# Optimization experiments

Hardware: AMD Instinct MI355X
Metric: run time of the kernel (lower is better)

## Reference

```python
import jax, jax.numpy as jnp
import numpy as np

D_MODEL = 1024
N_HEAD = 16
B, T = 4, 1024
MAX_REL = 32  # max_relative_positions


def setup_inputs() -> dict:
    key = jax.random.key(0)
    ks = jax.random.split(key, 12)
    s = 0.02
    inp = {
        "x": jax.random.normal(ks[0], (B, T, D_MODEL), jnp.float32),
        "mask": jnp.tril(jnp.ones((T, T), dtype=bool)),  # causal mask, 1 = keep
        "Wq": jax.random.normal(ks[1], (D_MODEL, D_MODEL), jnp.float32) * s,
        "bq": jax.random.normal(ks[2], (D_MODEL,), jnp.float32) * s,
        "Wk": jax.random.normal(ks[3], (D_MODEL, D_MODEL), jnp.float32) * s,
        "bk": jax.random.normal(ks[4], (D_MODEL,), jnp.float32) * s,
        "Wv": jax.random.normal(ks[5], (D_MODEL, D_MODEL), jnp.float32) * s,
        "bv": jax.random.normal(ks[6], (D_MODEL,), jnp.float32) * s,
        "Wo": jax.random.normal(ks[7], (D_MODEL, D_MODEL), jnp.float32) * s,
        "bo": jax.random.normal(ks[8], (D_MODEL,), jnp.float32) * s,
        "rel_bias": jax.random.normal(ks[9], (2 * MAX_REL - 1, N_HEAD), jnp.float32) * s,
        "n_head": N_HEAD,
    }
    return inp


def reference(x, mask, Wq, bq, Wk, bk, Wv, bv, Wo, bo, rel_bias, n_head):
    Bx, Tx, C = x.shape
    Dh = C // n_head
    scale = Dh ** (-0.5)
    # projections: torch Linear is x @ W.T + b
    Q = (x @ Wq.T + bq).reshape(Bx, Tx, n_head, Dh)
    K = (x @ Wk.T + bk).reshape(Bx, Tx, n_head, Dh)
    V = (x @ Wv.T + bv).reshape(Bx, Tx, n_head, Dh)
    # scores: [B, H, T, T]
    scores = jnp.einsum("bqhd,bkhd->bhqk", Q, K) * scale
    # T5-style clipped relative-position bias
    pos = jnp.arange(Tx)
    rel = pos[None, :] - pos[:, None]                     # k_pos - q_pos, [T, T]
    buckets = jnp.clip(rel, -(MAX_REL - 1), MAX_REL - 1) + (MAX_REL - 1)
    bias = rel_bias[buckets]                              # [T, T, H]
    scores = scores + jnp.transpose(bias, (2, 0, 1))[None]
    # original applies masked_fill(-inf) then masked_fill(0): net effect = 0
    scores = jnp.where(mask, scores, 0.0)
    w = jax.nn.relu(scores) + 1e-6
    w = jnp.where(mask, w, 0.0)
    w = w / (jnp.sum(w, axis=-1, keepdims=True) + 1e-6)
    out = jnp.einsum("bhqk,bkhd->bqhd", w, V).reshape(Bx, Tx, C)
    return out @ Wo.T + bo
```

## Files before the change

### kernel.cpp

```cpp
#include <hip/hip_runtime.h>


typedef __attribute__((ext_vector_type(8))) __bf16 bf16x8;
typedef __attribute__((ext_vector_type(4))) __bf16 bf16x4;
typedef __attribute__((ext_vector_type(4))) float f32x4;
typedef unsigned short u16;

__device__ __forceinline__ u16 f2bf(float f) {
  unsigned u = __float_as_uint(f);
  u += 0x7FFFu + ((u >> 16) & 1u);
  return (u16)(u >> 16);
}
__device__ __forceinline__ float bf2f(u16 b) {
  return __uint_as_float(((unsigned)b) << 16);
}
__device__ __forceinline__ void gl_lds16(const void* g, void* l) {
  __builtin_amdgcn_global_load_lds((__attribute__((address_space(1))) void*)g,
                                   (__attribute__((address_space(3))) void*)l,
                                   16, 0, 0);
}

__global__ __launch_bounds__(256) void cast_all_kernel(
    const float* __restrict__ x,  const float* __restrict__ wq,
    const float* __restrict__ wk, const float* __restrict__ wv,
    const float* __restrict__ wo,
    u16* __restrict__ xb, u16* __restrict__ wqb, u16* __restrict__ wkb,
    u16* __restrict__ wvb, u16* __restrict__ wob) {
  long i4 = (long)blockIdx.x * 256 + threadIdx.x;
  const float* src; u16* dst; long rel;
  if (i4 < 1048576) { src = x; dst = xb; rel = i4; }
  else {
    long j = i4 - 1048576;
    int w = (int)(j >> 18);
    rel = j & 262143;
    src = (w == 0) ? wq : (w == 1) ? wk : (w == 2) ? wv : wo;
    dst = (w == 0) ? wqb : (w == 1) ? wkb : (w == 2) ? wvb : wob;
  }
  float4 v = ((const float4*)src)[rel];
  ushort4 o;
  o.x = f2bf(v.x); o.y = f2bf(v.y); o.z = f2bf(v.z); o.w = f2bf(v.w);
  ((ushort4*)dst)[rel] = o;
}

__global__ __launch_bounds__(256) void gemm_qkv(
    const u16* __restrict__ xb, const u16* __restrict__ wqb,
    const u16* __restrict__ wkb, const u16* __restrict__ wvb,
    const float* __restrict__ bq, const float* __restrict__ bk,
    const float* __restrict__ bv,
    u16* __restrict__ Qb, u16* __restrict__ Kb, u16* __restrict__ Vtg) {
  constexpr int K = 1024;
  __shared__ __align__(16) u16 As[128 * 64];
  __shared__ __align__(16) u16 Bs[128 * 64];

  const int bx = blockIdx.x;
  const u16 *AT, *BT;
  const float* bias;
  u16* C;
  int m0, n0, ldc;
  bool rowbias;
  if (bx < 512) {
    int g = bx >> 5;
    int sel = g >> 3;
    n0 = (g & 7) * 128; m0 = (bx & 31) * 128;
    AT = xb; BT = sel ? wkb : wqb; bias = sel ? bk : bq;
    C = sel ? Kb : Qb; ldc = 1024; rowbias = false;
  } else {
    int rem = bx - 512;
    n0 = (rem >> 3) * 128; m0 = (rem & 7) * 128;
    AT = wvb; BT = xb; bias = bv;
    C = Vtg; ldc = 4096; rowbias = true;
  }

  const int t = threadIdx.x;
  const int lane = t & 63;
  const int wv = t >> 6;
  const int quad = lane >> 4;
  const int l15 = lane & 15;
  const int wr = wv >> 1, wc = wv & 1;

  const f32x4 vzero = {0.f, 0.f, 0.f, 0.f};
  f32x4 acc[4][4];
#pragma unroll
  for (int i = 0; i < 4; ++i)
#pragma unroll
    for (int j = 0; j < 4; ++j) acc[i][j] = vzero;

  for (int kt = 0; kt < K / 64; ++kt) {
    const int k0 = kt * 64;
#pragma unroll
    for (int p = 0; p < 4; ++p) {
      int idx = t + p * 256;
      int row = idx >> 3, seg = idx & 7;
      gl_lds16(&AT[(long)(m0 + row) * K + k0 + seg * 8], &As[idx * 8]);
      gl_lds16(&BT[(long)(n0 + row) * K + k0 + seg * 8], &Bs[idx * 8]);
    }
    __syncthreads();
#pragma unroll
    for (int ks = 0; ks < 64; ks += 32) {
      bf16x8 af[4], bfg[4];
#pragma unroll
      for (int i = 0; i < 4; ++i)
        af[i] = *(const bf16x8*)&As[(wr * 64 + i * 16 + l15) * 64 + ks + quad * 8];
#pragma unroll
      for (int j = 0; j < 4; ++j)
        bfg[j] = *(const bf16x8*)&Bs[(wc * 64 + j * 16 + l15) * 64 + ks + quad * 8];
#pragma unroll
      for (int i = 0; i < 4; ++i)
#pragma unroll
        for (int j = 0; j < 4; ++j)
          acc[i][j] = __builtin_amdgcn_mfma_f32_16x16x32_bf16(af[i], bfg[j], acc[i][j], 0, 0, 0);
    }
    __syncthreads();
  }

  float cb[4];
  if (!rowbias) {
#pragma unroll
    for (int j = 0; j < 4; ++j) cb[j] = bias[n0 + wc * 64 + j * 16 + l15];
  }

#pragma unroll
  for (int i = 0; i < 4; ++i) {
#pragma unroll
    for (int r = 0; r < 4; ++r) {
      int row = m0 + wr * 64 + i * 16 + quad * 4 + r;
      long base = (long)row * ldc + n0 + wc * 64;
      float rb_ = rowbias ? bias[row] : 0.f;
#pragma unroll
      for (int j = 0; j < 4; ++j) {
        float v = acc[i][j][r] + (rowbias ? rb_ : cb[j]);
        C[base + j * 16 + l15] = f2bf(v);
      }
    }
  }
}

__global__ __launch_bounds__(256) void gemm_out(
    const u16* __restrict__ A, const u16* __restrict__ B,
    const float* __restrict__ bias, float* __restrict__ C) {
  constexpr int K = 1024;
  __shared__ __align__(16) u16 As[128 * 64];
  __shared__ __align__(16) u16 Bs[128 * 64];

  const int m0 = blockIdx.x * 128;
  const int n0 = blockIdx.y * 128;

  const int t = threadIdx.x;
  const int lane = t & 63;
  const int wv = t >> 6;
  const int quad = lane >> 4;
  const int l15 = lane & 15;
  const int wr = wv >> 1, wc = wv & 1;

  const f32x4 vzero = {0.f, 0.f, 0.f, 0.f};
  f32x4 acc[4][4];
#pragma unroll
  for (int i = 0; i < 4; ++i)
#pragma unroll
    for (int j = 0; j < 4; ++j) acc[i][j] = vzero;

  for (int kt = 0; kt < K / 64; ++kt) {
    const int k0 = kt * 64;
#pragma unroll
    for (int p = 0; p < 4; ++p) {
      int idx = t + p * 256;
      int row = idx >> 3, seg = idx & 7;
      gl_lds16(&A[(long)(m0 + row) * K + k0 + seg * 8], &As[idx * 8]);
      gl_lds16(&B[(long)(n0 + row) * K + k0 + seg * 8], &Bs[idx * 8]);
    }
    __syncthreads();
#pragma unroll
    for (int ks = 0; ks < 64; ks += 32) {
      bf16x8 af[4], bfg[4];
#pragma unroll
      for (int i = 0; i < 4; ++i)
        af[i] = *(const bf16x8*)&As[(wr * 64 + i * 16 + l15) * 64 + ks + quad * 8];
#pragma unroll
      for (int j = 0; j < 4; ++j)
        bfg[j] = *(const bf16x8*)&Bs[(wc * 64 + j * 16 + l15) * 64 + ks + quad * 8];
#pragma unroll
      for (int i = 0; i < 4; ++i)
#pragma unroll
        for (int j = 0; j < 4; ++j)
          acc[i][j] = __builtin_amdgcn_mfma_f32_16x16x32_bf16(af[i], bfg[j], acc[i][j], 0, 0, 0);
    }
    __syncthreads();
  }

  float cb[4];
#pragma unroll
  for (int j = 0; j < 4; ++j) cb[j] = bias[n0 + wc * 64 + j * 16 + l15];

#pragma unroll
  for (int i = 0; i < 4; ++i) {
#pragma unroll
    for (int r = 0; r < 4; ++r) {
      int row = m0 + wr * 64 + i * 16 + quad * 4 + r;
      long base = (long)row * 1024 + n0 + wc * 64;
#pragma unroll
      for (int j = 0; j < 4; ++j)
        C[base + j * 16 + l15] = acc[i][j][r] + cb[j];
    }
  }
}

__global__ __launch_bounds__(256) void attn_split(
    const u16* __restrict__ Qb,
    const u16* __restrict__ Kb,
    const u16* __restrict__ Vtg,
    const float* __restrict__ rel_bias,
    u16* __restrict__ att,
    u16* __restrict__ Opart,
    float* __restrict__ Dpart) {
  constexpr int WS = 68;
  __shared__ __align__(16) u16 Kt[64 * 64];
  __shared__ __align__(16) u16 Vt[64 * 64];
  __shared__ __align__(16) u16 Ws[4][16 * WS];
  __shared__ float biasl[64];

  const int bx = blockIdx.x;
  const int bh = bx / 24;
  const int slot = bx - bh * 24;
  const int b = bh >> 4, h = bh & 15;

  int qb, cbeg, cend, pidx;
  bool multi;
  if (slot < 8) { qb = slot; cbeg = 0; cend = qb; multi = false; pidx = 0; }
  else {
    int s = slot - 8;
    qb = 8 + (s >> 1);
    int part = s & 1;
    multi = true;
    pidx = (bh * 8 + (qb - 8)) * 2 + part;
    if (part == 0) { cbeg = 0; cend = 7; }
    else           { cbeg = 8; cend = qb; }
  }
  const int q0 = qb * 64;

  const int t = threadIdx.x;
  const int lane = t & 63;
  const int wv = t >> 6;
  const int quad = lane >> 4;
  const int l15 = lane & 15;

  if (t < 63) biasl[t] = rel_bias[t * 16 + h];
  const float b0c = rel_bias[h];

  const long qrow = (long)(b * 1024 + q0 + wv * 16 + l15) * 1024 + h * 64;
  bf16x8 qf0 = *(const bf16x8*)&Qb[qrow + quad * 8];
  bf16x8 qf1 = *(const bf16x8*)&Qb[qrow + 32 + quad * 8];

  const f32x4 vzero = {0.f, 0.f, 0.f, 0.f};
  f32x4 acc_o[4];
#pragma unroll
  for (int j = 0; j < 4; ++j) acc_o[j] = vzero;
  float denom = 0.f;
  const float scale = 0.125f;
  const int ql = q0 + wv * 16 + l15;
  const int sw0 = (quad ^ (l15 & 7)) * 8;
  const int sw1 = ((4 + quad) ^ (l15 & 7)) * 8;

  for (int c = cbeg; c <= cend; ++c) {
    const int k0 = c * 64;
    if (c != cbeg) __syncthreads();
#pragma unroll
    for (int p = 0; p < 2; ++p) {
      int idx = t + p * 256;
      int row = idx >> 3, seg = idx & 7;
      int sw = row * 64 + ((seg ^ (row & 7)) * 8);
      uint4 kv = *(const uint4*)&Kb[(long)(b * 1024 + k0 + row) * 1024 + h * 64 + seg * 8];
      uint4 vv = *(const uint4*)&Vtg[(long)(h * 64 + row) * 4096 + b * 1024 + k0 + seg * 8];
      *(uint4*)&Kt[sw] = kv;
      *(uint4*)&Vt[sw] = vv;
    }
    __syncthreads();

    const bool fast = (c <= qb - 2);
#pragma unroll
    for (int g = 0; g < 4; ++g) {
      const u16* kr = &Kt[(g * 16 + l15) * 64];
      bf16x8 kf0 = *(const bf16x8*)&kr[sw0];
      bf16x8 kf1 = *(const bf16x8*)&kr[sw1];
      f32x4 sT = vzero;
      sT = __builtin_amdgcn_mfma_f32_16x16x32_bf16(kf0, qf0, sT, 0, 0, 0);
      sT = __builtin_amdgcn_mfma_f32_16x16x32_bf16(kf1, qf1, sT, 0, 0, 0);
      const int kgb = k0 + g * 16 + quad * 4;
      ushort4 wpk;
      if (fast) {
#pragma unroll
        for (int r = 0; r < 4; ++r) {
          float w = fmaxf(sT[r] * scale + b0c, 0.f) + 1e-6f;
          u16 wb = f2bf(w);
          denom += bf2f(wb);
          ((u16*)&wpk)[r] = wb;
        }
      } else {
#pragma unroll
        for (int r = 0; r < 4; ++r) {
          int kg = kgb + r;
          int dd = kg - ql;
          dd = dd < -31 ? -31 : (dd > 31 ? 31 : dd);
          float sv = sT[r] * scale + biasl[dd + 31];
          float w = (kg <= ql) ? (fmaxf(sv, 0.f) + 1e-6f) : 0.f;
          u16 wb = f2bf(w);
          denom += bf2f(wb);
          ((u16*)&wpk)[r] = wb;
        }
      }
      *(ushort4*)&Ws[wv][l15 * WS + g * 16 + quad * 4] = wpk;
    }
    asm volatile("s_waitcnt lgkmcnt(0)" ::: "memory");
#pragma unroll
    for (int ks = 0; ks < 64; ks += 32) {
      union { bf16x8 v8; bf16x4 v4[2]; } au;
      int wbase = l15 * WS + ks + quad * 8;
      au.v4[0] = *(const bf16x4*)&Ws[wv][wbase];
      au.v4[1] = *(const bf16x4*)&Ws[wv][wbase + 4];
      const int sv = ks ? sw1 : sw0;
#pragma unroll
      for (int j = 0; j < 4; ++j) {
        bf16x8 bvv = *(const bf16x8*)&Vt[(j * 16 + l15) * 64 + sv];
        acc_o[j] = __builtin_amdgcn_mfma_f32_16x16x32_bf16(au.v8, bvv, acc_o[j], 0, 0, 0);
      }
    }
  }

  denom += __shfl_xor(denom, 16);
  denom += __shfl_xor(denom, 32);

  if (!multi) {
    float invm = 1.f / (denom + 1e-6f);
    float inv[4];
#pragma unroll
    for (int r = 0; r < 4; ++r) inv[r] = __shfl(invm, quad * 4 + r);
#pragma unroll
    for (int j = 0; j < 4; ++j)
#pragma unroll
      for (int r = 0; r < 4; ++r) {
        int q = q0 + wv * 16 + quad * 4 + r;
        att[(long)(b * 1024 + q) * 1024 + h * 64 + j * 16 + l15] = f2bf(acc_o[j][r] * inv[r]);
      }
  } else {
    const int qrel = wv * 16 + quad * 4;
#pragma unroll
    for (int j = 0; j < 4; ++j)
#pragma unroll
      for (int r = 0; r < 4; ++r)
        Opart[(long)pidx * 4096 + (qrel + r) * 64 + j * 16 + l15] = f2bf(acc_o[j][r]);
    if (quad == 0) Dpart[pidx * 64 + wv * 16 + l15] = denom;
  }
}

__global__ __launch_bounds__(256) void attn_reduce(
    const u16* __restrict__ Opart, const float* __restrict__ Dpart,
    u16* __restrict__ att) {
  const int bx = blockIdx.x;
  const int bh = bx >> 3;
  const int q8 = bx & 7;
  const int b = bh >> 4, h = bh & 15;
  const int qb = 8 + q8;
  const int pidx = (bh * 8 + q8) * 2;

  const int t = threadIdx.x;
  const int row = t >> 2;
  const int dseg = t & 3;

  const float d0 = Dpart[pidx * 64 + row];
  const float d1 = Dpart[(pidx + 1) * 64 + row];
  const float inv = 1.f / (d0 + d1 + 1e-6f);

  const u16* O0 = Opart + (long)pidx * 4096 + row * 64 + dseg * 16;
  const u16* O1 = O0 + 4096;
  union { uint4 q[2]; u16 s[16]; } a, c, o;
  a.q[0] = *(const uint4*)O0;       a.q[1] = *(const uint4*)(O0 + 8);
  c.q[0] = *(const uint4*)O1;       c.q[1] = *(const uint4*)(O1 + 8);
#pragma unroll
  for (int i = 0; i < 16; ++i) o.s[i] = f2bf((bf2f(a.s[i]) + bf2f(c.s[i])) * inv);
  u16* dst = att + (long)(b * 1024 + qb * 64 + row) * 1024 + h * 64 + dseg * 16;
  *(uint4*)dst = o.q[0];
  *(uint4*)(dst + 8) = o.q[1];
}

extern "C" void kernel_launch(void* const* d_in, const int* in_sizes, int n_in,
                              void* d_out, int out_size, void* d_ws, size_t ws_size,
                              hipStream_t stream) {
  const float* x  = (const float*)d_in[0];
  const float* Wq = (const float*)d_in[2];
  const float* bq = (const float*)d_in[3];
  const float* Wk = (const float*)d_in[4];
  const float* bk = (const float*)d_in[5];
  const float* Wv = (const float*)d_in[6];
  const float* bv = (const float*)d_in[7];
  const float* Wo = (const float*)d_in[8];
  const float* bo = (const float*)d_in[9];
  const float* rb = (const float*)d_in[10];

  char* ws = (char*)d_ws;
  u16* xb      = (u16*)(ws);
  u16* Opart   = (u16*)(ws);
  u16* wqb     = (u16*)(ws + (8l  << 20));
  float* Dpart = (float*)(ws + (8l << 20));
  u16* wkb     = (u16*)(ws + (10l << 20));
  u16* wvb     = (u16*)(ws + (12l << 20));
  u16* wob     = (u16*)(ws + (14l << 20));
  u16* Qb      = (u16*)(ws + (16l << 20));
  u16* Kb      = (u16*)d_out;
  u16* Vtg     = (u16*)((char*)d_out + (8l << 20));

  cast_all_kernel<<<8192, 256, 0, stream>>>(x, Wq, Wk, Wv, Wo, xb, wqb, wkb, wvb, wob);
  gemm_qkv<<<768, 256, 0, stream>>>(xb, wqb, wkb, wvb, bq, bk, bv, Qb, Kb, Vtg);
  attn_split<<<1536, 256, 0, stream>>>(Qb, Kb, Vtg, rb, Qb, Opart, Dpart);
  attn_reduce<<<512, 256, 0, stream>>>(Opart, Dpart, Qb);
  gemm_out<<<dim3(32, 8), 256, 0, stream>>>(Qb, wob, bo, (float*)d_out);
}
```

Before: 203.0 us.

## Double-buffer GEMM LDS tiles and register-prefetch K/V chunks in attention

```diff
diff --git a/kernel.cpp b/kernel.cpp
--- a/kernel.cpp
+++ b/kernel.cpp
@@ -42,16 +42,97 @@
   ((ushort4*)dst)[rel] = o;
 }
 
+template <bool STORE_BF16>
+__device__ __forceinline__ void gemm_body(
+    const u16* __restrict__ A, const u16* __restrict__ B,
+    const float* __restrict__ bias, bool rowbias,
+    void* __restrict__ Cout, int ldc, int m0, int n0) {
+  constexpr int K = 1024;
+  constexpr int NT = K / 64;
+  __shared__ __align__(16) u16 As[2][128 * 64];
+  __shared__ __align__(16) u16 Bs[2][128 * 64];
+
+  const int t = threadIdx.x;
+  const int lane = t & 63;
+  const int wv = t >> 6;
+  const int quad = lane >> 4;
+  const int l15 = lane & 15;
+  const int wr = wv >> 1, wc = wv & 1;
+
+  const f32x4 vzero = {0.f, 0.f, 0.f, 0.f};
+  f32x4 acc[4][4];
+#pragma unroll
+  for (int i = 0; i < 4; ++i)
+#pragma unroll
+    for (int j = 0; j < 4; ++j) acc[i][j] = vzero;
+
+  auto stage = [&](int kt, int bufi) {
+#pragma unroll
+    for (int p = 0; p < 4; ++p) {
+      int idx = t + p * 256;
+      int row = idx >> 3, seg = idx & 7;
+      gl_lds16(&A[(long)(m0 + row) * K + kt * 64 + seg * 8], &As[bufi][idx * 8]);
+      gl_lds16(&B[(long)(n0 + row) * K + kt * 64 + seg * 8], &Bs[bufi][idx * 8]);
+    }
+  };
+
+  stage(0, 0);
+  for (int kt = 0; kt < NT; ++kt) {
+    const int bufi = kt & 1;
+    if (kt + 1 < NT) {
+      stage(kt + 1, bufi ^ 1);
+      asm volatile("s_waitcnt vmcnt(8)" ::: "memory");
+    } else {
+      asm volatile("s_waitcnt vmcnt(0)" ::: "memory");
+    }
+    asm volatile("s_barrier" ::: "memory");
+#pragma unroll
+    for (int ks = 0; ks < 64; ks += 32) {
+      bf16x8 af[4], bfg[4];
+#pragma unroll
+      for (int i = 0; i < 4; ++i)
+        af[i] = *(const bf16x8*)&As[bufi][(wr * 64 + i * 16 + l15) * 64 + ks + quad * 8];
+#pragma unroll
+      for (int j = 0; j < 4; ++j)
+        bfg[j] = *(const bf16x8*)&Bs[bufi][(wc * 64 + j * 16 + l15) * 64 + ks + quad * 8];
+#pragma unroll
+      for (int i = 0; i < 4; ++i)
+#pragma unroll
+        for (int j = 0; j < 4; ++j)
+          acc[i][j] = __builtin_amdgcn_mfma_f32_16x16x32_bf16(af[i], bfg[j], acc[i][j], 0, 0, 0);
+    }
+    asm volatile("s_barrier" ::: "memory");
+  }
+
+  float cb[4];
+  if (!rowbias) {
+#pragma unroll
+    for (int j = 0; j < 4; ++j) cb[j] = bias[n0 + wc * 64 + j * 16 + l15];
+  }
+
+#pragma unroll
+  for (int i = 0; i < 4; ++i) {
+#pragma unroll
+    for (int r = 0; r < 4; ++r) {
+      int row = m0 + wr * 64 + i * 16 + quad * 4 + r;
+      long base = (long)row * ldc + n0 + wc * 64;
+      float rb_ = rowbias ? bias[row] : 0.f;
+#pragma unroll
+      for (int j = 0; j < 4; ++j) {
+        float v = acc[i][j][r] + (rowbias ? rb_ : cb[j]);
+        if (STORE_BF16) ((u16*)Cout)[base + j * 16 + l15] = f2bf(v);
+        else            ((float*)Cout)[base + j * 16 + l15] = v;
+      }
+    }
+  }
+}
+
 __global__ __launch_bounds__(256) void gemm_qkv(
     const u16* __restrict__ xb, const u16* __restrict__ wqb,
     const u16* __restrict__ wkb, const u16* __restrict__ wvb,
     const float* __restrict__ bq, const float* __restrict__ bk,
     const float* __restrict__ bv,
     u16* __restrict__ Qb, u16* __restrict__ Kb, u16* __restrict__ Vtg) {
-  constexpr int K = 1024;
-  __shared__ __align__(16) u16 As[128 * 64];
-  __shared__ __align__(16) u16 Bs[128 * 64];
-
   const int bx = blockIdx.x;
   const u16 *AT, *BT;
   const float* bias;
@@ -70,138 +151,13 @@
     AT = wvb; BT = xb; bias = bv;
     C = Vtg; ldc = 4096; rowbias = true;
   }
-
-  const int t = threadIdx.x;
-  const int lane = t & 63;
-  const int wv = t >> 6;
-  const int quad = lane >> 4;
-  const int l15 = lane & 15;
-  const int wr = wv >> 1, wc = wv & 1;
-
-  const f32x4 vzero = {0.f, 0.f, 0.f, 0.f};
-  f32x4 acc[4][4];
-#pragma unroll
-  for (int i = 0; i < 4; ++i)
-#pragma unroll
-    for (int j = 0; j < 4; ++j) acc[i][j] = vzero;
-
-  for (int kt = 0; kt < K / 64; ++kt) {
-    const int k0 = kt * 64;
-#pragma unroll
-    for (int p = 0; p < 4; ++p) {
-      int idx = t + p * 256;
-      int row = idx >> 3, seg = idx & 7;
-      gl_lds16(&AT[(long)(m0 + row) * K + k0 + seg * 8], &As[idx * 8]);
-      gl_lds16(&BT[(long)(n0 + row) * K + k0 + seg * 8], &Bs[idx * 8]);
-    }
-    __syncthreads();
-#pragma unroll
-    for (int ks = 0; ks < 64; ks += 32) {
-      bf16x8 af[4], bfg[4];
-#pragma unroll
-      for (int i = 0; i < 4; ++i)
-        af[i] = *(const bf16x8*)&As[(wr * 64 + i * 16 + l15) * 64 + ks + quad * 8];
-#pragma unroll
-      for (int j = 0; j < 4; ++j)
-        bfg[j] = *(const bf16x8*)&Bs[(wc * 64 + j * 16 + l15) * 64 + ks + quad * 8];
-#pragma unroll
-      for (int i = 0; i < 4; ++i)
-#pragma unroll
-        for (int j = 0; j < 4; ++j)
-          acc[i][j] = __builtin_amdgcn_mfma_f32_16x16x32_bf16(af[i], bfg[j], acc[i][j], 0, 0, 0);
-    }
-    __syncthreads();
-  }
-
-  float cb[4];
-  if (!rowbias) {
-#pragma unroll
-    for (int j = 0; j < 4; ++j) cb[j] = bias[n0 + wc * 64 + j * 16 + l15];
-  }
-
-#pragma unroll
-  for (int i = 0; i < 4; ++i) {
-#pragma unroll
-    for (int r = 0; r < 4; ++r) {
-      int row = m0 + wr * 64 + i * 16 + quad * 4 + r;
-      long base = (long)row * ldc + n0 + wc * 64;
-      float rb_ = rowbias ? bias[row] : 0.f;
-#pragma unroll
-      for (int j = 0; j < 4; ++j) {
-        float v = acc[i][j][r] + (rowbias ? rb_ : cb[j]);
-        C[base + j * 16 + l15] = f2bf(v);
-      }
-    }
-  }
+  gemm_body<true>(AT, BT, bias, rowbias, C, ldc, m0, n0);
 }
 
 __global__ __launch_bounds__(256) void gemm_out(
     const u16* __restrict__ A, const u16* __restrict__ B,
     const float* __restrict__ bias, float* __restrict__ C) {
-  constexpr int K = 1024;
-  __shared__ __align__(16) u16 As[128 * 64];
-  __shared__ __align__(16) u16 Bs[128 * 64];
-
-  const int m0 = blockIdx.x * 128;
-  const int n0 = blockIdx.y * 128;
-
-  const int t = threadIdx.x;
-  const int lane = t & 63;
-  const int wv = t >> 6;
-  const int quad = lane >> 4;
-  const int l15 = lane & 15;
-  const int wr = wv >> 1, wc = wv & 1;
-
-  const f32x4 vzero = {0.f, 0.f, 0.f, 0.f};
-  f32x4 acc[4][4];
-#pragma unroll
-  for (int i = 0; i < 4; ++i)
-#pragma unroll
-    for (int j = 0; j < 4; ++j) acc[i][j] = vzero;
-
-  for (int kt = 0; kt < K / 64; ++kt) {
-    const int k0 = kt * 64;
-#pragma unroll
-    for (int p = 0; p < 4; ++p) {
-      int idx = t + p * 256;
-      int row = idx >> 3, seg = idx & 7;
-      gl_lds16(&A[(long)(m0 + row) * K + k0 + seg * 8], &As[idx * 8]);
-      gl_lds16(&B[(long)(n0 + row) * K + k0 + seg * 8], &Bs[idx * 8]);
-    }
-    __syncthreads();
-#pragma unroll
-    for (int ks = 0; ks < 64; ks += 32) {
-      bf16x8 af[4], bfg[4];
-#pragma unroll
-      for (int i = 0; i < 4; ++i)
-        af[i] = *(const bf16x8*)&As[(wr * 64 + i * 16 + l15) * 64 + ks + quad * 8];
-#pragma unroll
-      for (int j = 0; j < 4; ++j)
-        bfg[j] = *(const bf16x8*)&Bs[(wc * 64 + j * 16 + l15) * 64 + ks + quad * 8];
-#pragma unroll
-      for (int i = 0; i < 4; ++i)
-#pragma unroll
-        for (int j = 0; j < 4; ++j)
-          acc[i][j] = __builtin_amdgcn_mfma_f32_16x16x32_bf16(af[i], bfg[j], acc[i][j], 0, 0, 0);
-    }
-    __syncthreads();
-  }
-
-  float cb[4];
-#pragma unroll
-  for (int j = 0; j < 4; ++j) cb[j] = bias[n0 + wc * 64 + j * 16 + l15];
-
-#pragma unroll
-  for (int i = 0; i < 4; ++i) {
-#pragma unroll
-    for (int r = 0; r < 4; ++r) {
-      int row = m0 + wr * 64 + i * 16 + quad * 4 + r;
-      long base = (long)row * 1024 + n0 + wc * 64;
-#pragma unroll
-      for (int j = 0; j < 4; ++j)
-        C[base + j * 16 + l15] = acc[i][j][r] + cb[j];
-    }
-  }
+  gemm_body<false>(A, B, bias, false, C, 1024, blockIdx.x * 128, blockIdx.y * 128);
 }
 
 __global__ __launch_bounds__(256) void attn_split(
@@ -260,20 +216,39 @@
   const int sw0 = (quad ^ (l15 & 7)) * 8;
   const int sw1 = ((4 + quad) ^ (l15 & 7)) * 8;
 
+  uint4 kreg[2], vreg[2];
+  {
+    const int k0 = cbeg * 64;
+#pragma unroll
+    for (int p = 0; p < 2; ++p) {
+      int idx = t + p * 256;
+      int row = idx >> 3, seg = idx & 7;
+      kreg[p] = *(const uint4*)&Kb[(long)(b * 1024 + k0 + row) * 1024 + h * 64 + seg * 8];
+      vreg[p] = *(const uint4*)&Vtg[(long)(h * 64 + row) * 4096 + b * 1024 + k0 + seg * 8];
+    }
+  }
+
   for (int c = cbeg; c <= cend; ++c) {
     const int k0 = c * 64;
-    if (c != cbeg) __syncthreads();
 #pragma unroll
     for (int p = 0; p < 2; ++p) {
       int idx = t + p * 256;
       int row = idx >> 3, seg = idx & 7;
       int sw = row * 64 + ((seg ^ (row & 7)) * 8);
-      uint4 kv = *(const uint4*)&Kb[(long)(b * 1024 + k0 + row) * 1024 + h * 64 + seg * 8];
-      uint4 vv = *(const uint4*)&Vtg[(long)(h * 64 + row) * 4096 + b * 1024 + k0 + seg * 8];
-      *(uint4*)&Kt[sw] = kv;
-      *(uint4*)&Vt[sw] = vv;
+      *(uint4*)&Kt[sw] = kreg[p];
+      *(uint4*)&Vt[sw] = vreg[p];
     }
     __syncthreads();
+    if (c < cend) {
+      const int k0n = k0 + 64;
+#pragma unroll
+      for (int p = 0; p < 2; ++p) {
+        int idx = t + p * 256;
+        int row = idx >> 3, seg = idx & 7;
+        kreg[p] = *(const uint4*)&Kb[(long)(b * 1024 + k0n + row) * 1024 + h * 64 + seg * 8];
+        vreg[p] = *(const uint4*)&Vtg[(long)(h * 64 + row) * 4096 + b * 1024 + k0n + seg * 8];
+      }
+    }
 
     const bool fast = (c <= qb - 2);
 #pragma unroll
@@ -323,6 +298,7 @@
         acc_o[j] = __builtin_amdgcn_mfma_f32_16x16x32_bf16(au.v8, bvv, acc_o[j], 0, 0, 0);
       }
     }
+    asm volatile("s_barrier" ::: "memory");
   }
 
   denom += __shfl_xor(denom, 16);
```

Measured after the change: 244.3 us. +20.3%, slower.
